# Kernel optimization log

Hardware: AMD Instinct MI355X
Metric: run time of the kernel (lower is better)

## Reference

```python
import jax, jax.numpy as jnp
import numpy as np

N, D0, D1, HID, OUT = 4096, 256, 128, 64, 16
R, M, K, PROJ = 3, 2, 2, 128  # meta-path rels, same-type rels, schema rels, attn hidden


def setup_inputs() -> dict:
    key = jax.random.key(0)
    ks = jax.random.split(key, 24)
    g = lambda i, shape, s: jax.random.normal(ks[i], shape, jnp.float32) * s
    return {
        "features0": g(0, (N, D0), 1.0),
        "features1": g(1, (N, D1), 1.0),
        # row-scale adjacencies so aggregated features stay O(1)
        "adj_same": jax.random.uniform(ks[2], (M, N, N), jnp.float32) / N,
        "adj_meta": jax.random.uniform(ks[3], (R, N, N), jnp.float32) / N,
        "adj_schema": jax.random.uniform(ks[4], (K, N, N), jnp.float32) / N,
        "Wm0": g(5, (D0, HID), D0 ** -0.5), "bm0": jnp.zeros((HID,), jnp.float32),
        "Wm1": g(6, (D1, HID), D1 ** -0.5), "bm1": jnp.zeros((HID,), jnp.float32),
        "Wa": g(7, (HID, PROJ), HID ** -0.5), "ba": jnp.zeros((PROJ,), jnp.float32),
        "qa": g(8, (PROJ,), PROJ ** -0.5),
        "ws": g(9, (HID, 1), HID ** -0.5),
        "Wc1": g(10, (HID, PROJ), HID ** -0.5), "bc1": jnp.zeros((PROJ,), jnp.float32),
        "wc2": g(11, (PROJ, 1), PROJ ** -0.5),
        "Wt1": g(12, (HID, PROJ), HID ** -0.5), "bt1": jnp.zeros((PROJ,), jnp.float32),
        "wt2": g(13, (PROJ, 1), PROJ ** -0.5),
        "Wp": g(14, (HID, OUT), HID ** -0.5), "bp": jnp.zeros((OUT,), jnp.float32),
    }


def reference(features0, features1, adj_same, adj_meta, adj_schema,
              Wm0, bm0, Wm1, bm1, Wa, ba, qa, ws, Wc1, bc1, wc2,
              Wt1, bt1, wt2, Wp, bp):
    # per-type feature mapping: tanh(Linear(x))
    h0 = jnp.tanh(features0 @ Wm0 + bm0)  # [N, HID]
    h1 = jnp.tanh(features1 @ Wm1 + bm1)  # [N, HID]

    # --- Dif_Classes_AGG: meta-path aggregation + semantic attention over R relations ---
    hr = jnp.tanh(jnp.einsum('rij,jd->rid', adj_meta, h0))        # [R, N, HID]
    s = jnp.mean(jnp.tanh(hr @ Wa + ba) @ qa, axis=1)             # [R]
    beta_r = jax.nn.softmax(s)                                    # [R]
    relation_agg = jnp.einsum('r,rnd->nd', beta_r, hr)            # [N, HID]

    # --- Weight_Schema: schema-matrix aggregation with per-node softmax over K ---
    zk = jnp.einsum('kij,jd->kid', adj_schema, h1)                # [K, N, HID]
    beta_k = jax.nn.softmax(jnp.squeeze(zk @ ws, -1), axis=0)     # [K, N]
    item_classes_agg = jnp.einsum('kn,knd->nd', beta_k, zk)       # [N, HID]

    # --- Classes_Relation_AGG: same-type (item-item) aggregation over M relations ---
    ym = jnp.tanh(jnp.einsum('mij,jd->mid', adj_same, item_classes_agg))  # [M, N, HID]
    wm = jnp.squeeze(jnp.tanh(ym @ Wc1 + bc1) @ wc2, -1)          # [M, N]
    beta_m = jax.nn.softmax(wm, axis=0)                           # [M, N]
    item_item = jnp.einsum('mn,mnd->nd', beta_m, ym)              # [N, HID]

    # --- AggAttention over the two module outputs ---
    Hs = jnp.stack([relation_agg, item_item], axis=1)             # [N, 2, HID]
    wt = jnp.squeeze(jnp.tanh(Hs @ Wt1 + bt1) @ wt2, -1)          # [N, 2]
    beta_t = jax.nn.softmax(wt, axis=1)[..., None]                # [N, 2, 1]
    H = jnp.sum(beta_t * Hs, axis=1)                              # [N, HID]

    return (H @ Wp + bp, H)
```

## Files before the change

kernel.cpp:

```cpp
#include <hip/hip_runtime.h>

#define NODES 4096

typedef float f32x4 __attribute__((ext_vector_type(4)));
typedef __bf16 bf16x8 __attribute__((ext_vector_type(8)));
typedef unsigned short u16x8 __attribute__((ext_vector_type(8)));
typedef unsigned short u16x4 __attribute__((ext_vector_type(4)));

__device__ __forceinline__ unsigned short f2bf(float x) {
    unsigned u = __builtin_bit_cast(unsigned, x);
    return (unsigned short)((u + 0x7fffu + ((u >> 16) & 1u)) >> 16);
}

__global__ __launch_bounds__(256) void prep_h(
    const float* __restrict__ f0, const float* __restrict__ f1,
    const float* __restrict__ Wm0, const float* __restrict__ bm0,
    const float* __restrict__ Wm1, const float* __restrict__ bm1,
    unsigned short* __restrict__ hT0, unsigned short* __restrict__ hT1)
{
    const int d = threadIdx.x & 63;
    int n = blockIdx.x * 4 + (threadIdx.x >> 6);
    n = __builtin_amdgcn_readfirstlane(n);
    const float* r0 = f0 + (size_t)n * 256;
    float a0 = bm0[d];
#pragma unroll 8
    for (int k = 0; k < 256; ++k) a0 = fmaf(r0[k], Wm0[k * 64 + d], a0);
    hT0[(size_t)d * NODES + n] = f2bf(tanhf(a0));
    const float* r1 = f1 + (size_t)n * 128;
    float a1 = bm1[d];
#pragma unroll 8
    for (int k = 0; k < 128; ++k) a1 = fmaf(r1[k], Wm1[k * 64 + d], a1);
    hT1[(size_t)d * NODES + n] = f2bf(tanhf(a1));
}

__global__ __launch_bounds__(256, 5) void adj_gemm(
    const float* __restrict__ A0, const float* __restrict__ A1,
    const float* __restrict__ A2, const float* __restrict__ A3,
    const float* __restrict__ A4,
    const unsigned short* __restrict__ hTa, const unsigned short* __restrict__ hTb,
    int split, float* __restrict__ outBase, unsigned tanhMask)
{
    constexpr int BK = 64;
    constexpr int NT = NODES / BK;
    __shared__ unsigned short Al[2][16 * BK];
    __shared__ unsigned short Bl[2][64 * BK];

    const int job = blockIdx.y;
    const float* adj = job == 0 ? A0 : job == 1 ? A1 : job == 2 ? A2 : job == 3 ? A3 : A4;
    const unsigned short* hT = (job < split) ? hTa : hTb;
    float* C = outBase + (size_t)job * (NODES * 64);
    const bool doTanh = (tanhMask >> job) & 1u;

    const int t = threadIdx.x;
    const int row0 = blockIdx.x * 16;

    const int ar = t >> 4, ak = (t & 15) * 4;
    const int br = t >> 2, bk = (t & 3) * 16;
    const float* ap = adj + (size_t)(row0 + ar) * NODES + ak;
    const unsigned short* bpt = hT + (size_t)br * NODES + bk;
    const int aoff  = ((ar * 128 + ak * 2) ^ ((ar & 7) << 4)) >> 1;
    const int boff0 = ((br * 128 + bk * 2) ^ ((br & 7) << 4)) >> 1;
    const int boff1 = ((br * 128 + bk * 2 + 16) ^ ((br & 7) << 4)) >> 1;

    const int lane = t & 63, wid = t >> 6;
    const int fr = lane & 15, fg = lane >> 4;
    const int c0 = wid * 16;
    int afo[2], bfo[2];
#pragma unroll
    for (int s = 0; s < 2; ++s) {
        const int kk = (s * 32 + fg * 8) * 2;
        afo[s] = ((fr * 128 + kk) ^ ((fr & 7) << 4)) >> 1;
        const int dr = c0 + fr;
        bfo[s] = ((dr * 128 + kk) ^ ((dr & 7) << 4)) >> 1;
    }

    f32x4 acc = {0.f, 0.f, 0.f, 0.f};

    f32x4 av = *(const f32x4*)ap;
    u16x8 bv0 = *(const u16x8*)bpt;
    u16x8 bv1 = *(const u16x8*)(bpt + 8);
    ap += BK; bpt += BK;
    {
        u16x4 pk = { f2bf(av[0]), f2bf(av[1]), f2bf(av[2]), f2bf(av[3]) };
        *(u16x4*)(&Al[0][aoff]) = pk;
        *(u16x8*)(&Bl[0][boff0]) = bv0;
        *(u16x8*)(&Bl[0][boff1]) = bv1;
    }
    __syncthreads();

    int cur = 0;
    for (int kt = 0; kt < NT; ++kt) {
        f32x4 na; u16x8 nb0, nb1;
        const bool more = (kt + 1 < NT);
        if (more) {
            na  = *(const f32x4*)ap;
            nb0 = *(const u16x8*)bpt;
            nb1 = *(const u16x8*)(bpt + 8);
            ap += BK; bpt += BK;
        }
#pragma unroll
        for (int s = 0; s < 2; ++s) {
            u16x8 a16 = *(const u16x8*)(&Al[cur][afo[s]]);
            u16x8 b16 = *(const u16x8*)(&Bl[cur][bfo[s]]);
            acc = __builtin_amdgcn_mfma_f32_16x16x32_bf16(
                __builtin_bit_cast(bf16x8, a16), __builtin_bit_cast(bf16x8, b16), acc, 0, 0, 0);
        }
        if (more) {
            const int nx = cur ^ 1;
            u16x4 pk = { f2bf(na[0]), f2bf(na[1]), f2bf(na[2]), f2bf(na[3]) };
            *(u16x4*)(&Al[nx][aoff]) = pk;
            *(u16x8*)(&Bl[nx][boff0]) = nb0;
            *(u16x8*)(&Bl[nx][boff1]) = nb1;
        }
        __syncthreads();
        cur ^= 1;
    }

    float* Cw = C + (size_t)(row0 + fg * 4) * 64 + c0 + fr;
#pragma unroll
    for (int j = 0; j < 4; ++j) {
        float v = acc[j];
        if (doTanh) v = tanhf(v);
        Cw[(size_t)j * 64] = v;
    }
}

__global__ __launch_bounds__(128) void stage_c(
    const float* __restrict__ agg, const float* __restrict__ Wa,
    const float* __restrict__ ba, const float* __restrict__ qa,
    const float* __restrict__ wsv, float* __restrict__ sacc,
    unsigned short* __restrict__ iccT)
{
    const int n = blockIdx.x;
    const int p = threadIdx.x;
    __shared__ float rs[3][2];
    __shared__ float ru[2][2];

    const float* h0p = agg + (size_t)n * 64;
    const float* h1p = agg + ((size_t)NODES + n) * 64;
    const float* h2p = agg + ((size_t)2 * NODES + n) * 64;
    float a0 = ba[p], a1 = a0, a2 = a0;
#pragma unroll 8
    for (int d = 0; d < 64; ++d) {
        float w = Wa[d * 128 + p];
        a0 = fmaf(h0p[d], w, a0);
        a1 = fmaf(h1p[d], w, a1);
        a2 = fmaf(h2p[d], w, a2);
    }
    float qv = qa[p];
    float v0 = tanhf(a0) * qv, v1 = tanhf(a1) * qv, v2 = tanhf(a2) * qv;

    const float* z0 = agg + ((size_t)3 * NODES + n) * 64;
    const float* z1 = agg + ((size_t)4 * NODES + n) * 64;
    float u0 = (p < 64) ? z0[p] * wsv[p] : 0.f;
    float u1 = (p < 64) ? z1[p] * wsv[p] : 0.f;

#pragma unroll
    for (int off = 32; off; off >>= 1) {
        v0 += __shfl_down(v0, off); v1 += __shfl_down(v1, off); v2 += __shfl_down(v2, off);
        u0 += __shfl_down(u0, off); u1 += __shfl_down(u1, off);
    }
    if ((p & 63) == 0) {
        int w = p >> 6;
        rs[0][w] = v0; rs[1][w] = v1; rs[2][w] = v2;
        ru[0][w] = u0; ru[1][w] = u1;
    }
    __syncthreads();
    if (p < 3) atomicAdd(&sacc[p], rs[p][0] + rs[p][1]);

    float U0 = ru[0][0] + ru[0][1];
    float U1 = ru[1][0] + ru[1][1];
    float mx = fmaxf(U0, U1);
    float e0 = expf(U0 - mx), e1 = expf(U1 - mx);
    float inv = 1.f / (e0 + e1);
    if (p < 64) {
        float icc = (e0 * z0[p] + e1 * z1[p]) * inv;
        iccT[(size_t)p * NODES + n] = f2bf(icc);
    }
}

__global__ __launch_bounds__(256) void finalize(
    const float* __restrict__ agg, const float* __restrict__ ym,
    const float* __restrict__ sacc,
    const float* __restrict__ Wc1, const float* __restrict__ bc1, const float* __restrict__ wc2,
    const float* __restrict__ Wt1, const float* __restrict__ bt1, const float* __restrict__ wt2,
    const float* __restrict__ Wp, const float* __restrict__ bp,
    float* __restrict__ out)
{
    __shared__ float sWc[64 * 128];
    __shared__ float sWp[64 * 16];
    __shared__ float sHs0[2][64], sHs1[2][64], sHv[2][64];
    __shared__ float rA[2][2], rB[2][2];

    const int t = threadIdx.x;
    for (int i = t; i < 64 * 128; i += 256) sWc[i] = Wc1[i];
    for (int i = t; i < 64 * 16; i += 256) sWp[i] = Wp[i];

    float s0 = sacc[0] * (1.f / NODES), s1 = sacc[1] * (1.f / NODES), s2 = sacc[2] * (1.f / NODES);
    float sm = fmaxf(s0, fmaxf(s1, s2));
    float b0 = expf(s0 - sm), b1 = expf(s1 - sm), b2 = expf(s2 - sm);
    float bi = 1.f / (b0 + b1 + b2);
    b0 *= bi; b1 *= bi; b2 *= bi;

    const int sub = t >> 7;
    const int p = t & 127;
    const int wiH = p >> 6;
    const float bcv = bc1[p], wcv = wc2[p], btv = bt1[p], wtv = wt2[p];
    __syncthreads();

    for (int it = 0; it < 8; ++it) {
        const int n = blockIdx.x * 16 + it * 2 + sub;
        const float* y0 = ym + (size_t)n * 64;
        const float* y1 = ym + ((size_t)NODES + n) * 64;
        if (p < 64) {
            sHs0[sub][p] = b0 * agg[(size_t)n * 64 + p]
                         + b1 * agg[((size_t)NODES + n) * 64 + p]
                         + b2 * agg[((size_t)2 * NODES + n) * 64 + p];
        }
        float ac0 = bcv, ac1 = bcv;
#pragma unroll 8
        for (int d = 0; d < 64; ++d) {
            float w = sWc[d * 128 + p];
            ac0 = fmaf(y0[d], w, ac0);
            ac1 = fmaf(y1[d], w, ac1);
        }
        float v0 = tanhf(ac0) * wcv, v1 = tanhf(ac1) * wcv;
#pragma unroll
        for (int off = 32; off; off >>= 1) { v0 += __shfl_down(v0, off); v1 += __shfl_down(v1, off); }
        if ((p & 63) == 0) { rA[sub][wiH] = v0; rB[sub][wiH] = v1; }
        __syncthreads();
        float wm0 = rA[sub][0] + rA[sub][1];
        float wm1 = rB[sub][0] + rB[sub][1];
        float mm = fmaxf(wm0, wm1);
        float g0 = expf(wm0 - mm), g1 = expf(wm1 - mm);
        float gi = 1.f / (g0 + g1);
        g0 *= gi; g1 *= gi;
        if (p < 64) sHs1[sub][p] = g0 * y0[p] + g1 * y1[p];
        __syncthreads();

        float at0 = btv, at1 = btv;
#pragma unroll 8
        for (int d = 0; d < 64; ++d) {
            float w = Wt1[d * 128 + p];
            at0 = fmaf(sHs0[sub][d], w, at0);
            at1 = fmaf(sHs1[sub][d], w, at1);
        }
        float q0 = tanhf(at0) * wtv, q1 = tanhf(at1) * wtv;
#pragma unroll
        for (int off = 32; off; off >>= 1) { q0 += __shfl_down(q0, off); q1 += __shfl_down(q1, off); }
        if ((p & 63) == 0) { rA[sub][wiH] = q0; rB[sub][wiH] = q1; }
        __syncthreads();
        float t0 = rA[sub][0] + rA[sub][1];
        float t1 = rB[sub][0] + rB[sub][1];
        float tm = fmaxf(t0, t1);
        float c0 = expf(t0 - tm), c1 = expf(t1 - tm);
        float ci = 1.f / (c0 + c1);
        c0 *= ci; c1 *= ci;
        if (p < 64) {
            float H = c0 * sHs0[sub][p] + c1 * sHs1[sub][p];
            sHv[sub][p] = H;
            out[(size_t)NODES * 16 + (size_t)n * 64 + p] = H;
        }
        __syncthreads();
        if (p < 16) {
            float a = bp[p];
#pragma unroll 8
            for (int d = 0; d < 64; ++d) a = fmaf(sHv[sub][d], sWp[d * 16 + p], a);
            out[(size_t)n * 16 + p] = a;
        }
        __syncthreads();
    }
}

extern "C" void kernel_launch(void* const* d_in, const int* in_sizes, int n_in,
                              void* d_out, int out_size, void* d_ws, size_t ws_size,
                              hipStream_t stream)
{
    const float* f0   = (const float*)d_in[0];
    const float* f1   = (const float*)d_in[1];
    const float* adjS = (const float*)d_in[2];
    const float* adjM = (const float*)d_in[3];
    const float* adjK = (const float*)d_in[4];
    const float* Wm0  = (const float*)d_in[5];
    const float* bm0  = (const float*)d_in[6];
    const float* Wm1  = (const float*)d_in[7];
    const float* bm1  = (const float*)d_in[8];
    const float* Wa   = (const float*)d_in[9];
    const float* ba   = (const float*)d_in[10];
    const float* qa   = (const float*)d_in[11];
    const float* wsv  = (const float*)d_in[12];
    const float* Wc1  = (const float*)d_in[13];
    const float* bc1  = (const float*)d_in[14];
    const float* wc2  = (const float*)d_in[15];
    const float* Wt1  = (const float*)d_in[16];
    const float* bt1  = (const float*)d_in[17];
    const float* wt2  = (const float*)d_in[18];
    const float* Wp   = (const float*)d_in[19];
    const float* bpv  = (const float*)d_in[20];
    float* out = (float*)d_out;

    char* ws = (char*)d_ws;
    unsigned short* hT0  = (unsigned short*)(ws);
    unsigned short* hT1  = (unsigned short*)(ws + (512u << 10));
    float* agg           = (float*)(ws + (1024u << 10));
    unsigned short* iccT = (unsigned short*)(ws + (6144u << 10));
    float* ym            = (float*)(ws + (6656u << 10));
    float* sacc          = (float*)(ws + (8704u << 10));

    hipMemsetAsync(sacc, 0, 64, stream);
    prep_h<<<dim3(1024), dim3(256), 0, stream>>>(f0, f1, Wm0, bm0, Wm1, bm1, hT0, hT1);

    const size_t NNs = (size_t)NODES * NODES;
    adj_gemm<<<dim3(256, 5), dim3(256), 0, stream>>>(
        adjM, adjM + NNs, adjM + 2 * NNs, adjK, adjK + NNs,
        hT0, hT1, 3, agg, 0x7u);
    stage_c<<<dim3(4096), dim3(128), 0, stream>>>(agg, Wa, ba, qa, wsv, sacc, iccT);
    adj_gemm<<<dim3(256, 2), dim3(256), 0, stream>>>(
        adjS, adjS + NNs, adjS, adjS, adjS,
        iccT, iccT, 5, ym, 0x3u);
    finalize<<<dim3(256), dim3(256), 0, stream>>>(
        agg, ym, sacc, Wc1, bc1, wc2, Wt1, bt1, wt2, Wp, bpv, out);
}
```

Baseline: 274.5 us.

## Rewrite adjacency GEMM as LDS-free split-K MFMA with register fragments

The adjacency GEMM no longer stages tiles through shared memory. Each wave now loads its A and B MFMA fragments straight from global memory and covers all 64 output columns with four accumulators. The K dimension is split across the four waves and combined with a shared-memory reduction, which removes the per-step barriers and LDS round trips. For the second GEMM (same-type adjacency), K is also split across two blocks that write partial sums, and finalize adds the partials and applies tanh. This raises per-thread register use and uncoalesced-looking strided fragment loads, and adds extra partial-sum traffic.

Measured after the change: 323.4 us. +17.8%, slower.

```diff
diff --git a/kernel.cpp b/kernel.cpp
--- a/kernel.cpp
+++ b/kernel.cpp
@@ -3,6 +3,7 @@
 #define NODES 4096
 
 typedef float f32x4 __attribute__((ext_vector_type(4)));
+typedef float f32x8 __attribute__((ext_vector_type(8)));
 typedef __bf16 bf16x8 __attribute__((ext_vector_type(8)));
 typedef unsigned short u16x8 __attribute__((ext_vector_type(8)));
 typedef unsigned short u16x4 __attribute__((ext_vector_type(4)));
@@ -38,90 +39,82 @@
     const float* __restrict__ A2, const float* __restrict__ A3,
     const float* __restrict__ A4,
     const unsigned short* __restrict__ hTa, const unsigned short* __restrict__ hTb,
-    int split, float* __restrict__ outBase, unsigned tanhMask)
-{
-    constexpr int BK = 64;
-    constexpr int NT = NODES / BK;
-    __shared__ unsigned short Al[2][16 * BK];
-    __shared__ unsigned short Bl[2][64 * BK];
+    int split, float* __restrict__ outBase, unsigned tanhMask,
+    int rgShift, int kcw)
+{
+    __shared__ float red[3][64][20];
 
     const int job = blockIdx.y;
     const float* adj = job == 0 ? A0 : job == 1 ? A1 : job == 2 ? A2 : job == 3 ? A3 : A4;
     const unsigned short* hT = (job < split) ? hTa : hTb;
-    float* C = outBase + (size_t)job * (NODES * 64);
     const bool doTanh = (tanhMask >> job) & 1u;
 
-    const int t = threadIdx.x;
-    const int row0 = blockIdx.x * 16;
-
-    const int ar = t >> 4, ak = (t & 15) * 4;
-    const int br = t >> 2, bk = (t & 3) * 16;
-    const float* ap = adj + (size_t)(row0 + ar) * NODES + ak;
-    const unsigned short* bpt = hT + (size_t)br * NODES + bk;
-    const int aoff  = ((ar * 128 + ak * 2) ^ ((ar & 7) << 4)) >> 1;
-    const int boff0 = ((br * 128 + bk * 2) ^ ((br & 7) << 4)) >> 1;
-    const int boff1 = ((br * 128 + bk * 2 + 16) ^ ((br & 7) << 4)) >> 1;
-
-    const int lane = t & 63, wid = t >> 6;
+    const int bx = blockIdx.x;
+    const int rg = bx >> rgShift;
+    const int kh = bx & ((1 << rgShift) - 1);
+    const int row0 = rg * 16;
+    const int lane = threadIdx.x & 63;
+    const int wid = threadIdx.x >> 6;
     const int fr = lane & 15, fg = lane >> 4;
-    const int c0 = wid * 16;
-    int afo[2], bfo[2];
-#pragma unroll
-    for (int s = 0; s < 2; ++s) {
-        const int kk = (s * 32 + fg * 8) * 2;
-        afo[s] = ((fr * 128 + kk) ^ ((fr & 7) << 4)) >> 1;
-        const int dr = c0 + fr;
-        bfo[s] = ((dr * 128 + kk) ^ ((dr & 7) << 4)) >> 1;
-    }
-
-    f32x4 acc = {0.f, 0.f, 0.f, 0.f};
-
-    f32x4 av = *(const f32x4*)ap;
-    u16x8 bv0 = *(const u16x8*)bpt;
-    u16x8 bv1 = *(const u16x8*)(bpt + 8);
-    ap += BK; bpt += BK;
-    {
-        u16x4 pk = { f2bf(av[0]), f2bf(av[1]), f2bf(av[2]), f2bf(av[3]) };
-        *(u16x4*)(&Al[0][aoff]) = pk;
-        *(u16x8*)(&Bl[0][boff0]) = bv0;
-        *(u16x8*)(&Bl[0][boff1]) = bv1;
+    const int kbeg = kh * (kcw * 4) + wid * kcw;
+    const int nkt = kcw >> 5;
+
+    const char* aB = (const char*)adj;
+    const char* hB = (const char*)hT;
+    unsigned aoff = (unsigned)(((row0 + fr) * NODES + kbeg + fg * 8) * 4);
+    unsigned boff = (unsigned)((fr * NODES + kbeg + fg * 8) * 2);
+    const unsigned bstep = NODES * 32u;
+
+    f32x8 aN = *(const f32x8*)(aB + aoff);
+    u16x8 bN0 = *(const u16x8*)(hB + boff);
+    u16x8 bN1 = *(const u16x8*)(hB + boff + bstep);
+    u16x8 bN2 = *(const u16x8*)(hB + boff + 2 * bstep);
+    u16x8 bN3 = *(const u16x8*)(hB + boff + 3 * bstep);
+    aoff += 128; boff += 64;
+
+    f32x4 acc0 = {0.f,0.f,0.f,0.f}, acc1 = {0.f,0.f,0.f,0.f};
+    f32x4 acc2 = {0.f,0.f,0.f,0.f}, acc3 = {0.f,0.f,0.f,0.f};
+
+    for (int kt = 0; kt < nkt; ++kt) {
+        f32x8 aC = aN;
+        u16x8 b0 = bN0, b1 = bN1, b2 = bN2, b3 = bN3;
+        if (kt + 1 < nkt) {
+            aN  = *(const f32x8*)(aB + aoff);
+            bN0 = *(const u16x8*)(hB + boff);
+            bN1 = *(const u16x8*)(hB + boff + bstep);
+            bN2 = *(const u16x8*)(hB + boff + 2 * bstep);
+            bN3 = *(const u16x8*)(hB + boff + 3 * bstep);
+            aoff += 128; boff += 64;
+        }
+        bf16x8 af = __builtin_convertvector(aC, bf16x8);
+        acc0 = __builtin_amdgcn_mfma_f32_16x16x32_bf16(af, __builtin_bit_cast(bf16x8, b0), acc0, 0, 0, 0);
+        acc1 = __builtin_amdgcn_mfma_f32_16x16x32_bf16(af, __builtin_bit_cast(bf16x8, b1), acc1, 0, 0, 0);
+        acc2 = __builtin_amdgcn_mfma_f32_16x16x32_bf16(af, __builtin_bit_cast(bf16x8, b2), acc2, 0, 0, 0);
+        acc3 = __builtin_amdgcn_mfma_f32_16x16x32_bf16(af, __builtin_bit_cast(bf16x8, b3), acc3, 0, 0, 0);
+    }
+
+    if (wid) {
+        float* r = &red[wid - 1][lane][0];
+        *(f32x4*)(r + 0)  = acc0; *(f32x4*)(r + 4)  = acc1;
+        *(f32x4*)(r + 8)  = acc2; *(f32x4*)(r + 12) = acc3;
     }
     __syncthreads();
-
-    int cur = 0;
-    for (int kt = 0; kt < NT; ++kt) {
-        f32x4 na; u16x8 nb0, nb1;
-        const bool more = (kt + 1 < NT);
-        if (more) {
-            na  = *(const f32x4*)ap;
-            nb0 = *(const u16x8*)bpt;
-            nb1 = *(const u16x8*)(bpt + 8);
-            ap += BK; bpt += BK;
-        }
-#pragma unroll
-        for (int s = 0; s < 2; ++s) {
-            u16x8 a16 = *(const u16x8*)(&Al[cur][afo[s]]);
-            u16x8 b16 = *(const u16x8*)(&Bl[cur][bfo[s]]);
-            acc = __builtin_amdgcn_mfma_f32_16x16x32_bf16(
-                __builtin_bit_cast(bf16x8, a16), __builtin_bit_cast(bf16x8, b16), acc, 0, 0, 0);
-        }
-        if (more) {
-            const int nx = cur ^ 1;
-            u16x4 pk = { f2bf(na[0]), f2bf(na[1]), f2bf(na[2]), f2bf(na[3]) };
-            *(u16x4*)(&Al[nx][aoff]) = pk;
-            *(u16x8*)(&Bl[nx][boff0]) = nb0;
-            *(u16x8*)(&Bl[nx][boff1]) = nb1;
-        }
-        __syncthreads();
-        cur ^= 1;
-    }
-
-    float* Cw = C + (size_t)(row0 + fg * 4) * 64 + c0 + fr;
-#pragma unroll
-    for (int j = 0; j < 4; ++j) {
-        float v = acc[j];
-        if (doTanh) v = tanhf(v);
-        Cw[(size_t)j * 64] = v;
+    if (wid == 0) {
+#pragma unroll
+        for (int w = 0; w < 3; ++w) {
+            const float* r = &red[w][lane][0];
+            acc0 += *(const f32x4*)(r + 0);  acc1 += *(const f32x4*)(r + 4);
+            acc2 += *(const f32x4*)(r + 8);  acc3 += *(const f32x4*)(r + 12);
+        }
+        float* C = outBase + (size_t)((job << rgShift) | kh) * (NODES * 64);
+        float* Cw = C + (size_t)(row0 + fg * 4) * 64 + fr;
+#pragma unroll
+        for (int j = 0; j < 4; ++j) {
+            float v0 = acc0[j], v1 = acc1[j], v2 = acc2[j], v3 = acc3[j];
+            if (doTanh) { v0 = tanhf(v0); v1 = tanhf(v1); v2 = tanhf(v2); v3 = tanhf(v3); }
+            Cw[j * 64 + 0]  = v0; Cw[j * 64 + 16] = v1;
+            Cw[j * 64 + 32] = v2; Cw[j * 64 + 48] = v3;
+        }
     }
 }
 
@@ -180,7 +173,7 @@
 }
 
 __global__ __launch_bounds__(256) void finalize(
-    const float* __restrict__ agg, const float* __restrict__ ym,
+    const float* __restrict__ agg, const float* __restrict__ ymp,
     const float* __restrict__ sacc,
     const float* __restrict__ Wc1, const float* __restrict__ bc1, const float* __restrict__ wc2,
     const float* __restrict__ Wt1, const float* __restrict__ bt1, const float* __restrict__ wt2,
@@ -189,6 +182,7 @@
 {
     __shared__ float sWc[64 * 128];
     __shared__ float sWp[64 * 16];
+    __shared__ float sY0[2][64], sY1[2][64];
     __shared__ float sHs0[2][64], sHs1[2][64], sHv[2][64];
     __shared__ float rA[2][2], rB[2][2];
 
@@ -210,19 +204,23 @@
 
     for (int it = 0; it < 8; ++it) {
         const int n = blockIdx.x * 16 + it * 2 + sub;
-        const float* y0 = ym + (size_t)n * 64;
-        const float* y1 = ym + ((size_t)NODES + n) * 64;
         if (p < 64) {
+            const size_t NN64 = (size_t)NODES * 64;
+            float ya = ymp[(size_t)n * 64 + p]          + ymp[NN64 + (size_t)n * 64 + p];
+            float yb = ymp[2 * NN64 + (size_t)n * 64 + p] + ymp[3 * NN64 + (size_t)n * 64 + p];
+            sY0[sub][p] = tanhf(ya);
+            sY1[sub][p] = tanhf(yb);
             sHs0[sub][p] = b0 * agg[(size_t)n * 64 + p]
                          + b1 * agg[((size_t)NODES + n) * 64 + p]
                          + b2 * agg[((size_t)2 * NODES + n) * 64 + p];
         }
+        __syncthreads();
         float ac0 = bcv, ac1 = bcv;
 #pragma unroll 8
         for (int d = 0; d < 64; ++d) {
             float w = sWc[d * 128 + p];
-            ac0 = fmaf(y0[d], w, ac0);
-            ac1 = fmaf(y1[d], w, ac1);
+            ac0 = fmaf(sY0[sub][d], w, ac0);
+            ac1 = fmaf(sY1[sub][d], w, ac1);
         }
         float v0 = tanhf(ac0) * wcv, v1 = tanhf(ac1) * wcv;
 #pragma unroll
@@ -235,7 +233,7 @@
         float g0 = expf(wm0 - mm), g1 = expf(wm1 - mm);
         float gi = 1.f / (g0 + g1);
         g0 *= gi; g1 *= gi;
-        if (p < 64) sHs1[sub][p] = g0 * y0[p] + g1 * y1[p];
+        if (p < 64) sHs1[sub][p] = g0 * sY0[sub][p] + g1 * sY1[sub][p];
         __syncthreads();
 
         float at0 = btv, at1 = btv;
@@ -301,11 +299,11 @@
 
     char* ws = (char*)d_ws;
     unsigned short* hT0  = (unsigned short*)(ws);
-    unsigned short* hT1  = (unsigned short*)(ws + (512u << 10));
-    float* agg           = (float*)(ws + (1024u << 10));
-    unsigned short* iccT = (unsigned short*)(ws + (6144u << 10));
-    float* ym            = (float*)(ws + (6656u << 10));
-    float* sacc          = (float*)(ws + (8704u << 10));
+    unsigned short* hT1  = (unsigned short*)(ws + 524288);
+    unsigned short* iccT = (unsigned short*)(ws + 1048576);
+    float* agg           = (float*)(ws + 1572864);
+    float* ymp           = (float*)(ws + 4718592);
+    float* sacc          = (float*)(ws + 8912896);
 
     hipMemsetAsync(sacc, 0, 64, stream);
     prep_h<<<dim3(1024), dim3(256), 0, stream>>>(f0, f1, Wm0, bm0, Wm1, bm1, hT0, hT1);
@@ -313,11 +311,11 @@
     const size_t NNs = (size_t)NODES * NODES;
     adj_gemm<<<dim3(256, 5), dim3(256), 0, stream>>>(
         adjM, adjM + NNs, adjM + 2 * NNs, adjK, adjK + NNs,
-        hT0, hT1, 3, agg, 0x7u);
+        hT0, hT1, 3, agg, 0x7u, 0, 1024);
     stage_c<<<dim3(4096), dim3(128), 0, stream>>>(agg, Wa, ba, qa, wsv, sacc, iccT);
-    adj_gemm<<<dim3(256, 2), dim3(256), 0, stream>>>(
+    adj_gemm<<<dim3(512, 2), dim3(256), 0, stream>>>(
         adjS, adjS + NNs, adjS, adjS, adjS,
-        iccT, iccT, 5, ym, 0x3u);
+        iccT, iccT, 5, ymp, 0x0u, 1, 512);
     finalize<<<dim3(256), dim3(256), 0, stream>>>(
-        agg, ym, sacc, Wc1, bc1, wc2, Wt1, bt1, wt2, Wp, bpv, out);
-}
+        agg, ymp, sacc, Wc1, bc1, wc2, Wt1, bt1, wt2, Wp, bpv, out);
+}
```
